# Kernel optimization log

Hardware: AMD Instinct MI355X
Metric: run time of the kernel (lower is better)

## Reference

```python
import jax, jax.numpy as jnp
import numpy as np

HID = 1024
HEADS = 16
HEAD_DIM = HID // HEADS
MAX_REL = 2


def _rel_embed(table, length_q, length_k):
    # table: [2*MAX_REL+1, head_dim] -> [len_q, len_k, head_dim]
    dist = jnp.arange(length_k)[None, :] - jnp.arange(length_q)[:, None]
    idx = jnp.clip(dist, -MAX_REL, MAX_REL) + MAX_REL
    return table[idx]


def setup_inputs() -> dict:
    key = jax.random.key(0)
    ks = jax.random.split(key, 16)
    B, S = 2, 2048
    bound = 1.0 / np.sqrt(HID)

    def lin(k1, k2):
        W = jax.random.uniform(k1, (HID, HID), jnp.float32, -bound, bound)
        b = jax.random.uniform(k2, (HID,), jnp.float32, -bound, bound)
        return W, b

    Wq, bq = lin(ks[0], ks[1])
    Wk, bk = lin(ks[2], ks[3])
    Wv, bv = lin(ks[4], ks[5])
    Wo, bo = lin(ks[6], ks[7])
    # xavier_uniform for [5, head_dim] tables
    xav = np.sqrt(6.0 / (2 * MAX_REL + 1 + HEAD_DIM))
    rel_k = jax.random.uniform(ks[8], (2 * MAX_REL + 1, HEAD_DIM), jnp.float32, -xav, xav)
    rel_v = jax.random.uniform(ks[9], (2 * MAX_REL + 1, HEAD_DIM), jnp.float32, -xav, xav)
    return {
        'key': jax.random.normal(ks[10], (B, S, HID), jnp.float32),
        'query': jax.random.normal(ks[11], (B, S, HID), jnp.float32),
        'value': jax.random.normal(ks[12], (B, S, HID), jnp.float32),
        'Wq': Wq, 'bq': bq, 'Wk': Wk, 'bk': bk, 'Wv': Wv, 'bv': bv,
        'Wo': Wo, 'bo': bo, 'rel_k': rel_k, 'rel_v': rel_v,
    }


def reference(key, query, value, Wq, bq, Wk, bk, Wv, bv, Wo, bo, rel_k, rel_v):
    B, Lq, _ = query.shape
    Lk = key.shape[1]
    q = query @ Wq.T + bq   # [B, Lq, HID]
    k = key @ Wk.T + bk     # [B, Lk, HID]
    v = value @ Wv.T + bv   # [B, Lk, HID]

    qh = q.reshape(B, Lq, HEADS, HEAD_DIM).transpose(0, 2, 1, 3)  # [B,H,Lq,D]
    kh = k.reshape(B, Lk, HEADS, HEAD_DIM).transpose(0, 2, 1, 3)
    vh = v.reshape(B, Lk, HEADS, HEAD_DIM).transpose(0, 2, 1, 3)

    attn1 = jnp.einsum('bhqd,bhkd->bhqk', qh, kh)
    rk = _rel_embed(rel_k, Lq, Lk)                                # [Lq,Lk,D]
    attn2 = jnp.einsum('bhqd,qkd->bhqk', qh, rk)
    scale = jnp.sqrt(jnp.float32(HEAD_DIM))
    attn = jax.nn.softmax((attn1 + attn2) / scale, axis=-1)      # [B,H,Lq,Lk]

    w1 = jnp.einsum('bhqk,bhkd->bhqd', attn, vh)
    rv = _rel_embed(rel_v, Lq, Lk)                                # [Lq,Lk,D]
    w2 = jnp.einsum('bhqk,qkd->bhqd', attn, rv)

    x = (w1 + w2).transpose(0, 2, 1, 3).reshape(B, Lq, HID)
    return x @ Wo.T + bo
```

## Files before the change

### kernel.cpp

```cpp
#include <hip/hip_runtime.h>
#include <hip/hip_bf16.h>

#define S_LEN 2048
#define HID_DIM 1024
#define NH 16
#define HD 64
#define MTOT 4096

typedef __attribute__((ext_vector_type(8))) short short8;
typedef __attribute__((ext_vector_type(4))) float f32x4;

__device__ __forceinline__ float bf2f(unsigned short u) {
  union { unsigned int i; float f; } x; x.i = ((unsigned int)u) << 16; return x.f;
}
__device__ __forceinline__ unsigned short f2bf(float f) {
  union { float ff; unsigned int i; } x; x.ff = f;
  return (unsigned short)((x.i + 0x7fffu + ((x.i >> 16) & 1u)) >> 16);
}
__device__ __forceinline__ unsigned short f2bf_rna(float f) {
  union { float ff; unsigned int i; } x; x.ff = f;
  return (unsigned short)((x.i + 0x8000u) >> 16);
}
__device__ __forceinline__ f32x4 mfma16(short8 a, short8 b, f32x4 c) {
  return __builtin_amdgcn_mfma_f32_16x16x32_bf16(a, b, c, 0, 0, 0);
}
__device__ __forceinline__ void gl_lds16(const unsigned short* g, unsigned short* l) {
  __builtin_amdgcn_global_load_lds(
      (const __attribute__((address_space(1))) unsigned int*)g,
      (__attribute__((address_space(3))) unsigned int*)l, 16, 0, 0);
}

__global__ __launch_bounds__(256) void cvt3(const float* __restrict__ a, const float* __restrict__ b,
                                            const float* __restrict__ c, unsigned short* __restrict__ oa,
                                            unsigned short* __restrict__ ob, unsigned short* __restrict__ oc,
                                            int n4) {
  int i = blockIdx.x * 256 + threadIdx.x;
  if (i >= n4) return;
  const float* src = blockIdx.y == 0 ? a : blockIdx.y == 1 ? b : c;
  unsigned short* dst = blockIdx.y == 0 ? oa : blockIdx.y == 1 ? ob : oc;
  float4 v = reinterpret_cast<const float4*>(src)[i];
  union { unsigned short u[4]; unsigned long long ll; } o;
  o.u[0] = f2bf(v.x); o.u[1] = f2bf(v.y); o.u[2] = f2bf(v.z); o.u[3] = f2bf(v.w);
  reinterpret_cast<unsigned long long*>(dst)[i] = o.ll;
}
__global__ __launch_bounds__(256) void cvt4(const float* __restrict__ a, const float* __restrict__ b,
                                            const float* __restrict__ c, const float* __restrict__ d,
                                            unsigned short* __restrict__ oa, unsigned short* __restrict__ ob,
                                            unsigned short* __restrict__ oc, unsigned short* __restrict__ od,
                                            int n4) {
  int i = blockIdx.x * 256 + threadIdx.x;
  if (i >= n4) return;
  const float* src = blockIdx.y == 0 ? a : blockIdx.y == 1 ? b : blockIdx.y == 2 ? c : d;
  unsigned short* dst = blockIdx.y == 0 ? oa : blockIdx.y == 1 ? ob : blockIdx.y == 2 ? oc : od;
  float4 v = reinterpret_cast<const float4*>(src)[i];
  union { unsigned short u[4]; unsigned long long ll; } o;
  o.u[0] = f2bf(v.x); o.u[1] = f2bf(v.y); o.u[2] = f2bf(v.z); o.u[3] = f2bf(v.w);
  reinterpret_cast<unsigned long long*>(dst)[i] = o.ll;
}

__device__ __forceinline__ void gemm_core(const unsigned short* __restrict__ A,
                                          const unsigned short* __restrict__ W,
                                          unsigned short* As, unsigned short* Bs,
                                          int m0, int n0, f32x4 (&acc)[4][4]) {
  const int tid = threadIdx.x;
  const int lane = tid & 63;
  const int wrow = (tid >> 6) >> 1, wcol = (tid >> 6) & 1;
  const int lr = lane & 15, g = lane >> 4;
  const int r32 = tid >> 3;
  const int cph = (tid & 7) ^ (r32 & 7);
  const unsigned short* ag = A + (size_t)(m0 + r32) * HID_DIM + cph * 8;
  const unsigned short* bg = W + (size_t)(n0 + r32) * HID_DIM + cph * 8;
  unsigned short* al = As + tid * 8;
  unsigned short* bl = Bs + tid * 8;
  for (int k0 = 0; k0 < HID_DIM; k0 += 64) {
    __syncthreads();
#pragma unroll
    for (int p = 0; p < 4; ++p) {
      gl_lds16(ag + (size_t)(p * 32) * HID_DIM + k0, al + p * 2048);
      gl_lds16(bg + (size_t)(p * 32) * HID_DIM + k0, bl + p * 2048);
    }
    __syncthreads();
#pragma unroll
    for (int ks = 0; ks < 2; ++ks) {
      short8 af[4], bfr[4];
#pragma unroll
      for (int m = 0; m < 4; ++m)
        af[m] = *reinterpret_cast<const short8*>(
            &As[(wrow * 64 + m * 16 + lr) * 64 + (((ks * 4 + g) ^ (lr & 7)) * 8)]);
#pragma unroll
      for (int n = 0; n < 4; ++n)
        bfr[n] = *reinterpret_cast<const short8*>(
            &Bs[(wcol * 64 + n * 16 + lr) * 64 + (((ks * 4 + g) ^ (lr & 7)) * 8)]);
#pragma unroll
      for (int m = 0; m < 4; ++m)
#pragma unroll
        for (int n = 0; n < 4; ++n)
          acc[m][n] = mfma16(af[m], bfr[n], acc[m][n]);
    }
  }
}

__global__ __launch_bounds__(256) void qkv_gemm(
    const unsigned short* __restrict__ Aq, const unsigned short* __restrict__ Ak,
    const unsigned short* __restrict__ Av,
    const unsigned short* __restrict__ Wq, const unsigned short* __restrict__ Wk,
    const unsigned short* __restrict__ Wv,
    const float* __restrict__ bq, const float* __restrict__ bk, const float* __restrict__ bv,
    unsigned short* __restrict__ Qp, unsigned short* __restrict__ Kp,
    unsigned short* __restrict__ Vt) {
  __shared__ __attribute__((aligned(16))) unsigned short As[128 * 64];
  __shared__ __attribute__((aligned(16))) unsigned short Bs[128 * 64];
  const int which = blockIdx.x >> 3;
  const int n0 = (blockIdx.x & 7) * 128;
  const int m0 = blockIdx.y * 128;
  const unsigned short* A = which == 0 ? Aq : which == 1 ? Ak : Av;
  const unsigned short* W = which == 0 ? Wq : which == 1 ? Wk : Wv;
  const float* bias = which == 0 ? bq : which == 1 ? bk : bv;

  f32x4 acc[4][4];
  const f32x4 vzero = {0.f, 0.f, 0.f, 0.f};
#pragma unroll
  for (int m = 0; m < 4; ++m)
#pragma unroll
    for (int n = 0; n < 4; ++n) acc[m][n] = vzero;

  gemm_core(A, W, As, Bs, m0, n0, acc);

  const int lane = threadIdx.x & 63;
  const int wrow = (threadIdx.x >> 6) >> 1, wcol = (threadIdx.x >> 6) & 1;
  const int lr = lane & 15, g = lane >> 4;
  const float scl = (which == 0) ? 0.125f : 1.0f;
#pragma unroll
  for (int m = 0; m < 4; ++m) {
    const int rbase = m0 + wrow * 64 + m * 16 + g * 4;
#pragma unroll
    for (int n = 0; n < 4; ++n) {
      const int col = n0 + wcol * 64 + n * 16 + lr;
      const float bcol = bias[col];
      if (which < 2) {
        unsigned short* O = which == 0 ? Qp : Kp;
#pragma unroll
        for (int rg = 0; rg < 4; ++rg)
          O[(size_t)(rbase + rg) * HID_DIM + col] = f2bf((acc[m][n][rg] + bcol) * scl);
      } else {
        const int bb = rbase >> 11, s = rbase & 2047;
        const int h = col >> 6, d = col & 63;
        union { unsigned short u[4]; unsigned long long ll; } o;
#pragma unroll
        for (int rg = 0; rg < 4; ++rg) o.u[rg] = f2bf(acc[m][n][rg] + bcol);
        *reinterpret_cast<unsigned long long*>(
            &Vt[((size_t)(bb * NH + h) * HD + d) * S_LEN + s]) = o.ll;
      }
    }
  }
}

__global__ __launch_bounds__(256) void out_gemm(const unsigned short* __restrict__ X,
                                                const unsigned short* __restrict__ Wo,
                                                const float* __restrict__ bo,
                                                float* __restrict__ out) {
  __shared__ __attribute__((aligned(16))) unsigned short As[128 * 64];
  __shared__ __attribute__((aligned(16))) unsigned short Bs[128 * 64];
  const int n0 = blockIdx.x * 128;
  const int m0 = blockIdx.y * 128;
  f32x4 acc[4][4];
  const f32x4 vzero = {0.f, 0.f, 0.f, 0.f};
#pragma unroll
  for (int m = 0; m < 4; ++m)
#pragma unroll
    for (int n = 0; n < 4; ++n) acc[m][n] = vzero;

  gemm_core(X, Wo, As, Bs, m0, n0, acc);

  const int lane = threadIdx.x & 63;
  const int wrow = (threadIdx.x >> 6) >> 1, wcol = (threadIdx.x >> 6) & 1;
  const int lr = lane & 15, g = lane >> 4;
#pragma unroll
  for (int m = 0; m < 4; ++m) {
    const int rbase = m0 + wrow * 64 + m * 16 + g * 4;
#pragma unroll
    for (int n = 0; n < 4; ++n) {
      const int col = n0 + wcol * 64 + n * 16 + lr;
      const float bcol = bo[col];
#pragma unroll
      for (int rg = 0; rg < 4; ++rg)
        out[(size_t)(rbase + rg) * HID_DIM + col] = acc[m][n][rg] + bcol;
    }
  }
}

__global__ __launch_bounds__(512, 2) void attn_kernel(
    const unsigned short* __restrict__ Qp, const unsigned short* __restrict__ Kp,
    const unsigned short* __restrict__ Vt, const float* __restrict__ relk,
    const float* __restrict__ relv, unsigned short* __restrict__ Xa) {
  __shared__ __attribute__((aligned(16))) unsigned short kv[2][8192];
  __shared__ __attribute__((aligned(16))) unsigned short Ps[8][16][72];
  __shared__ float projs[128][5];
  __shared__ float relks[5][64];
  __shared__ float rvs[5][64];

  const int tid = threadIdx.x;
  const int lane = tid & 63;
  const int w = tid >> 6;
  const int lr = lane & 15, g = lane >> 4;
  const int virt = (blockIdx.x & 7) * 64 + (blockIdx.x >> 3);
  const int bh = virt >> 4;
  const int qbase = (virt & 15) * 128;
  const int b = bh >> 4, h = bh & 15;

  const unsigned short* Qg = Qp + ((size_t)(b * S_LEN + qbase)) * HID_DIM + h * HD;
  const unsigned short* Kg = Kp + ((size_t)b * S_LEN) * HID_DIM + h * HD;
  const unsigned short* Vg = Vt + (size_t)bh * HD * S_LEN;

#pragma unroll
  for (int i = 0; i < 2; ++i) {
    const int flat = i * 8192 + tid * 16;
    const int row = flat >> 7, c = (flat >> 4) & 7;
    gl_lds16(Qg + (size_t)row * HID_DIM + ((c ^ (row & 7)) * 8), &kv[1][flat >> 1]);
  }
  {
    const int flat = tid * 16;
    const int row = flat >> 7, c = (flat >> 4) & 7;
    const int csrc = (c ^ (row & 7)) * 8;
    gl_lds16(Kg + (size_t)row * HID_DIM + csrc, &kv[0][flat >> 1]);
    gl_lds16(Vg + (size_t)row * S_LEN + csrc, &kv[0][4096 + (flat >> 1)]);
  }
  for (int i = tid; i < 320; i += 512) {
    ((float*)relks)[i] = relk[i];
    ((float*)rvs)[i] = relv[i];
  }
  __syncthreads();

  for (int idx = tid; idx < 640; idx += 512) {
    const int row = idx & 127, j = idx >> 7;
    float acc = 0.f;
    for (int d = 0; d < 64; ++d)
      acc += bf2f(kv[1][row * 64 + ((d >> 3) ^ (row & 7)) * 8 + (d & 7)]) * relks[j][d];
    projs[row][j] = acc;
  }
  short8 aq[2];
#pragma unroll
  for (int h2 = 0; h2 < 2; ++h2) {
    const int row = w * 16 + lr;
    aq[h2] = *reinterpret_cast<const short8*>(
        &kv[1][row * 64 + (((g + 4 * h2) ^ (lr & 7)) * 8)]);
  }
  __syncthreads();

  float pj0[4], pj4[4];
#pragma unroll
  for (int i = 0; i < 4; ++i) {
    const int qloc = w * 16 + g * 4 + i;
    pj0[i] = projs[qloc][0];
    pj4[i] = projs[qloc][4];
  }
  f32x4 cinitL, cinitR;
#pragma unroll
  for (int i = 0; i < 4; ++i) { cinitL[i] = pj0[i]; cinitR[i] = pj4[i]; }

  const f32x4 vzero = {0.f, 0.f, 0.f, 0.f};
  f32x4 accO[4];
#pragma unroll
  for (int n = 0; n < 4; ++n) accO[n] = vzero;
  float sp0[4], sp4[4], sv1[4], sv2[4], sv3[4];
#pragma unroll
  for (int i = 0; i < 4; ++i) {
    sp0[i] = 0.f; sp4[i] = 0.f; sv1[i] = 0.f; sv2[i] = 0.f; sv3[i] = 0.f;
  }
  const int Qw = qbase + w * 16;

  for (int t = 0; t < 32; ++t) {
    const int kb = t * 64;
    const unsigned short* Ks = kv[t & 1];
    const unsigned short* Vs = Ks + 4096;
    if (t < 31) {
      const int kb2 = kb + 64;
      unsigned short* dst = &kv[(t + 1) & 1][0];
      const int flat = tid * 16;
      const int row = flat >> 7, c = (flat >> 4) & 7;
      const int csrc = (c ^ (row & 7)) * 8;
      gl_lds16(Kg + (size_t)(kb2 + row) * HID_DIM + csrc, dst + (flat >> 1));
      gl_lds16(Vg + (size_t)row * S_LEN + kb2 + csrc, dst + 4096 + (flat >> 1));
    }
    const bool mixed = (kb + 63 >= Qw - 2) && (kb <= Qw + 17);
    const bool left = kb < Qw;
    const f32x4 ci = mixed ? vzero : (left ? cinitL : cinitR);
    short8 kf[4][2];
#pragma unroll
    for (int n = 0; n < 4; ++n)
#pragma unroll
      for (int h2 = 0; h2 < 2; ++h2)
        kf[n][h2] = *reinterpret_cast<const short8*>(
            &Ks[(n * 16 + lr) * 64 + (((g + 4 * h2) ^ (lr & 7)) * 8)]);
    f32x4 accS[4];
#pragma unroll
    for (int n = 0; n < 4; ++n) {
      f32x4 z = mfma16(aq[0], kf[n][0], ci);
      accS[n] = mfma16(aq[1], kf[n][1], z);
    }

    if (!mixed) {
#pragma unroll
      for (int n = 0; n < 4; ++n)
#pragma unroll
        for (int r = 0; r < 4; ++r) {
          const float p = __expf(accS[n][r]);
          if (left) sp0[r] += p; else sp4[r] += p;
          Ps[w][g * 4 + r][n * 16 + lr] = f2bf_rna(p);
        }
    } else {
#pragma unroll
      for (int n = 0; n < 4; ++n) {
        const int kg = kb + n * 16 + lr;
#pragma unroll
        for (int r = 0; r < 4; ++r) {
          const int qloc = w * 16 + g * 4 + r;
          const int dist = kg - (qbase + qloc);
          float pjv;
          if (dist <= -2) pjv = pj0[r];
          else if (dist >= 2) pjv = pj4[r];
          else pjv = projs[qloc][dist + 2];
          const float p = __expf(accS[n][r] + pjv);
          if (dist <= -2) sp0[r] += p;
          else if (dist >= 2) sp4[r] += p;
          else if (dist == -1) sv1[r] += p;
          else if (dist == 0) sv2[r] += p;
          else sv3[r] += p;
          Ps[w][g * 4 + r][n * 16 + lr] = f2bf_rna(p);
        }
      }
    }
    asm volatile("" ::: "memory");
    short8 vf[4][2];
#pragma unroll
    for (int n = 0; n < 4; ++n)
#pragma unroll
      for (int h2 = 0; h2 < 2; ++h2)
        vf[n][h2] = *reinterpret_cast<const short8*>(
            &Vs[(n * 16 + lr) * 64 + (((g + 4 * h2) ^ (lr & 7)) * 8)]);
    short8 pa0 = *reinterpret_cast<const short8*>(&Ps[w][lr][g * 8]);
    short8 pa1 = *reinterpret_cast<const short8*>(&Ps[w][lr][g * 8 + 32]);
#pragma unroll
    for (int n = 0; n < 4; ++n) {
      accO[n] = mfma16(pa0, vf[n][0], accO[n]);
      accO[n] = mfma16(pa1, vf[n][1], accO[n]);
    }
    __syncthreads();
  }

#pragma unroll
  for (int i = 0; i < 4; ++i) {
    float v0 = sp0[i], v1 = sv1[i], v2 = sv2[i], v3 = sv3[i], v4 = sp4[i];
#pragma unroll
    for (int s = 1; s <= 8; s <<= 1) {
      v0 += __shfl_xor(v0, s); v1 += __shfl_xor(v1, s); v2 += __shfl_xor(v2, s);
      v3 += __shfl_xor(v3, s); v4 += __shfl_xor(v4, s);
    }
    const float rl = 1.f / (v0 + v1 + v2 + v3 + v4);
    const int qrow = b * S_LEN + qbase + w * 16 + g * 4 + i;
#pragma unroll
    for (int n = 0; n < 4; ++n) {
      const int d = n * 16 + lr;
      const float val = (accO[n][i] + v0 * rvs[0][d] + v1 * rvs[1][d] +
                         v2 * rvs[2][d] + v3 * rvs[3][d] + v4 * rvs[4][d]) * rl;
      Xa[(size_t)qrow * HID_DIM + h * HD + d] = f2bf(val);
    }
  }
}

extern "C" void kernel_launch(void* const* d_in, const int* in_sizes, int n_in,
                              void* d_out, int out_size, void* d_ws, size_t ws_size,
                              hipStream_t stream) {
  (void)in_sizes; (void)n_in; (void)out_size; (void)ws_size;
  const float* f_key   = (const float*)d_in[0];
  const float* f_query = (const float*)d_in[1];
  const float* f_value = (const float*)d_in[2];
  const float* Wq = (const float*)d_in[3];
  const float* bq = (const float*)d_in[4];
  const float* Wk = (const float*)d_in[5];
  const float* bk = (const float*)d_in[6];
  const float* Wv = (const float*)d_in[7];
  const float* bv = (const float*)d_in[8];
  const float* Wo = (const float*)d_in[9];
  const float* bo = (const float*)d_in[10];
  const float* relk = (const float*)d_in[11];
  const float* relv = (const float*)d_in[12];

  char* ws = (char*)d_ws;
  const size_t SZ = (size_t)MTOT * HID_DIM * sizeof(unsigned short);
  unsigned short* cq  = (unsigned short*)(ws + 0 * SZ);
  unsigned short* ck  = (unsigned short*)(ws + 1 * SZ);
  unsigned short* cv  = (unsigned short*)(ws + 2 * SZ);
  unsigned short* wqb = (unsigned short*)(ws + 3 * SZ);
  unsigned short* wkb = wqb + 1024 * 1024;
  unsigned short* wvb = wkb + 1024 * 1024;
  unsigned short* wob = wvb + 1024 * 1024;
  unsigned short* Qp  = (unsigned short*)(ws + 4 * SZ);
  unsigned short* Kp  = (unsigned short*)(ws + 5 * SZ);
  unsigned short* Vt  = (unsigned short*)(ws + 6 * SZ);
  unsigned short* xa  = cq;

  const int nIn4 = MTOT * HID_DIM / 4;
  const int nW4 = 1024 * 1024 / 4;
  cvt3<<<dim3(nIn4 / 256, 3), 256, 0, stream>>>(f_query, f_key, f_value, cq, ck, cv, nIn4);
  cvt4<<<dim3(nW4 / 256, 4), 256, 0, stream>>>(Wq, Wk, Wv, Wo, wqb, wkb, wvb, wob, nW4);
  qkv_gemm<<<dim3(24, 32), dim3(256), 0, stream>>>(cq, ck, cv, wqb, wkb, wvb, bq, bk, bv,
                                                   Qp, Kp, Vt);
  attn_kernel<<<dim3(512), dim3(512), 0, stream>>>(Qp, Kp, Vt, relk, relv, xa);
  out_gemm<<<dim3(8, 32), dim3(256), 0, stream>>>(xa, wob, bo, (float*)d_out);
}
```

Baseline: 153.5 us.

## Read V fragments directly from global memory and use exp2 softmax

Stops staging V tiles through LDS: the double-buffered LDS region now holds only K, and each wave loads its V MFMA fragments straight from global/L2 inside the key loop. Separately, the Q projection scale now includes log2(e), so the softmax can use exp2f instead of __expf. The V change cuts LDS traffic and footprint. In exchange, all eight waves redundantly fetch the same V tile from global memory, and that load latency now sits directly on the inner loop with no prefetch.

```diff
diff --git a/kernel.cpp b/kernel.cpp
--- a/kernel.cpp
+++ b/kernel.cpp
@@ -129,7 +129,7 @@
   const int lane = threadIdx.x & 63;
   const int wrow = (threadIdx.x >> 6) >> 1, wcol = (threadIdx.x >> 6) & 1;
   const int lr = lane & 15, g = lane >> 4;
-  const float scl = (which == 0) ? 0.125f : 1.0f;
+  const float scl = (which == 0) ? 0.125f * 1.44269504f : 1.0f;
 #pragma unroll
   for (int m = 0; m < 4; ++m) {
     const int rbase = m0 + wrow * 64 + m * 16 + g * 4;
@@ -193,7 +193,7 @@
     const unsigned short* __restrict__ Qp, const unsigned short* __restrict__ Kp,
     const unsigned short* __restrict__ Vt, const float* __restrict__ relk,
     const float* __restrict__ relv, unsigned short* __restrict__ Xa) {
-  __shared__ __attribute__((aligned(16))) unsigned short kv[2][8192];
+  __shared__ __attribute__((aligned(16))) unsigned short kv[2][4096];
   __shared__ __attribute__((aligned(16))) unsigned short Ps[8][16][72];
   __shared__ float projs[128][5];
   __shared__ float relks[5][64];
@@ -211,19 +211,13 @@
   const unsigned short* Qg = Qp + ((size_t)(b * S_LEN + qbase)) * HID_DIM + h * HD;
   const unsigned short* Kg = Kp + ((size_t)b * S_LEN) * HID_DIM + h * HD;
   const unsigned short* Vg = Vt + (size_t)bh * HD * S_LEN;
+  unsigned short* kvf = &kv[0][0];
 
 #pragma unroll
   for (int i = 0; i < 2; ++i) {
     const int flat = i * 8192 + tid * 16;
     const int row = flat >> 7, c = (flat >> 4) & 7;
-    gl_lds16(Qg + (size_t)row * HID_DIM + ((c ^ (row & 7)) * 8), &kv[1][flat >> 1]);
-  }
-  {
-    const int flat = tid * 16;
-    const int row = flat >> 7, c = (flat >> 4) & 7;
-    const int csrc = (c ^ (row & 7)) * 8;
-    gl_lds16(Kg + (size_t)row * HID_DIM + csrc, &kv[0][flat >> 1]);
-    gl_lds16(Vg + (size_t)row * S_LEN + csrc, &kv[0][4096 + (flat >> 1)]);
+    gl_lds16(Qg + (size_t)row * HID_DIM + ((c ^ (row & 7)) * 8), kvf + (flat >> 1));
   }
   for (int i = tid; i < 320; i += 512) {
     ((float*)relks)[i] = relk[i];
@@ -235,7 +229,7 @@
     const int row = idx & 127, j = idx >> 7;
     float acc = 0.f;
     for (int d = 0; d < 64; ++d)
-      acc += bf2f(kv[1][row * 64 + ((d >> 3) ^ (row & 7)) * 8 + (d & 7)]) * relks[j][d];
+      acc += bf2f(kvf[row * 64 + ((d >> 3) ^ (row & 7)) * 8 + (d & 7)]) * relks[j][d];
     projs[row][j] = acc;
   }
   short8 aq[2];
@@ -243,7 +237,14 @@
   for (int h2 = 0; h2 < 2; ++h2) {
     const int row = w * 16 + lr;
     aq[h2] = *reinterpret_cast<const short8*>(
-        &kv[1][row * 64 + (((g + 4 * h2) ^ (lr & 7)) * 8)]);
+        &kvf[row * 64 + (((g + 4 * h2) ^ (lr & 7)) * 8)]);
+  }
+  __syncthreads();
+
+  {
+    const int flat = tid * 16;
+    const int row = flat >> 7, c = (flat >> 4) & 7;
+    gl_lds16(Kg + (size_t)row * HID_DIM + ((c ^ (row & 7)) * 8), &kv[0][flat >> 1]);
   }
   __syncthreads();
 
@@ -272,15 +273,11 @@
   for (int t = 0; t < 32; ++t) {
     const int kb = t * 64;
     const unsigned short* Ks = kv[t & 1];
-    const unsigned short* Vs = Ks + 4096;
     if (t < 31) {
-      const int kb2 = kb + 64;
-      unsigned short* dst = &kv[(t + 1) & 1][0];
       const int flat = tid * 16;
       const int row = flat >> 7, c = (flat >> 4) & 7;
-      const int csrc = (c ^ (row & 7)) * 8;
-      gl_lds16(Kg + (size_t)(kb2 + row) * HID_DIM + csrc, dst + (flat >> 1));
-      gl_lds16(Vg + (size_t)row * S_LEN + kb2 + csrc, dst + 4096 + (flat >> 1));
+      gl_lds16(Kg + (size_t)(kb + 64 + row) * HID_DIM + ((c ^ (row & 7)) * 8),
+               &kv[(t + 1) & 1][flat >> 1]);
     }
     const bool mixed = (kb + 63 >= Qw - 2) && (kb <= Qw + 17);
     const bool left = kb < Qw;
@@ -304,7 +301,7 @@
       for (int n = 0; n < 4; ++n)
 #pragma unroll
         for (int r = 0; r < 4; ++r) {
-          const float p = __expf(accS[n][r]);
+          const float p = exp2f(accS[n][r]);
           if (left) sp0[r] += p; else sp4[r] += p;
           Ps[w][g * 4 + r][n * 16 + lr] = f2bf_rna(p);
         }
@@ -320,7 +317,7 @@
           if (dist <= -2) pjv = pj0[r];
           else if (dist >= 2) pjv = pj4[r];
           else pjv = projs[qloc][dist + 2];
-          const float p = __expf(accS[n][r] + pjv);
+          const float p = exp2f(accS[n][r] + pjv);
           if (dist <= -2) sp0[r] += p;
           else if (dist >= 2) sp4[r] += p;
           else if (dist == -1) sv1[r] += p;
@@ -333,11 +330,11 @@
     asm volatile("" ::: "memory");
     short8 vf[4][2];
 #pragma unroll
-    for (int n = 0; n < 4; ++n)
-#pragma unroll
-      for (int h2 = 0; h2 < 2; ++h2)
-        vf[n][h2] = *reinterpret_cast<const short8*>(
-            &Vs[(n * 16 + lr) * 64 + (((g + 4 * h2) ^ (lr & 7)) * 8)]);
+    for (int n = 0; n < 4; ++n) {
+      const unsigned short* vp = Vg + (size_t)(n * 16 + lr) * S_LEN + kb + g * 8;
+      vf[n][0] = *reinterpret_cast<const short8*>(vp);
+      vf[n][1] = *reinterpret_cast<const short8*>(vp + 32);
+    }
     short8 pa0 = *reinterpret_cast<const short8*>(&Ps[w][lr][g * 8]);
     short8 pa1 = *reinterpret_cast<const short8*>(&Ps[w][lr][g * 8 + 32]);
 #pragma unroll
```

After: 267.1 us. 1.74x slower.
